# Performance work log

Hardware: AMD Instinct MI355X
Metric: run time of the kernel (lower is better)

The kernel has to match this reference:

```python
import jax, jax.numpy as jnp
import numpy as np

N_HEADS = 12
HEAD_DIM = 32
H_OUT = 28
W_OUT = 28
EPS_LN = 1e-6
EPS_TS = 1e-6


def _layer_norm(x, g, eps=EPS_LN):
    mu = jnp.mean(x, axis=-1, keepdims=True)
    xc = x - mu
    var = jnp.mean(xc * xc, axis=-1, keepdims=True)
    return xc * jax.lax.rsqrt(var + eps) * g


def setup_inputs() -> dict:
    key = jax.random.key(0)
    ks = jax.random.split(key, 6)
    b, hh, ww, d = 4, 56, 56, 384
    nc = 2 * H_OUT * W_OUT  # 1568
    s = 0.02
    return {
        "x": jax.random.normal(ks[0], (b, hh, ww, d), jnp.float32),
        "clusters": jax.random.normal(ks[1], (b, nc, d), jnp.float32),
        "g1": jnp.ones((d,), jnp.float32),
        "Wq": jax.random.normal(ks[2], (d, d), jnp.float32) * s,
        "Wkv": jax.random.normal(ks[3], (d, 2 * d), jnp.float32) * s,
        "Wo": jax.random.normal(ks[4], (d, d), jnp.float32) * s,
        "res_scale": jnp.ones((d,), jnp.float32),
        "g2": jnp.ones((2 * d,), jnp.float32),
        "Wproj": jax.random.normal(ks[5], (2 * d, 768), jnp.float32) * s,
    }


def reference(x, clusters, g1, Wq, Wkv, Wo, res_scale, g2, Wproj):
    b, hh, ww, d = x.shape
    n = hh * ww
    nc = clusters.shape[1]
    dh = HEAD_DIM
    scale = dh ** -0.5

    xf = x.reshape(b, n, d)
    xn = _layer_norm(xf, g1)
    cn = _layer_norm(clusters, g1)

    # projections; rearrange 'b n (h d) -> b h n d' and 'b n (k h d) -> k b h n d'
    q = (cn @ Wq).reshape(b, nc, N_HEADS, dh).transpose(0, 2, 1, 3)
    kv = (xn @ Wkv).reshape(b, n, 2, N_HEADS, dh)
    k = kv[:, :, 0].transpose(0, 2, 1, 3)  # [b h n dh]
    v = kv[:, :, 1].transpose(0, 2, 1, 3)

    attn = jnp.einsum('bhqd,bhkd->bhqk', q, k) * scale  # [b h nc n]
    # soft assignment: softmax over the query (cluster) axis
    attn = jax.nn.softmax(attn, axis=-2)
    token_sizes = attn.sum(-1)  # [b h nc]
    attn = attn / (token_sizes[..., None] + EPS_TS)
    token_sizes = token_sizes.mean(1)  # [b nc]

    c2 = jnp.einsum('bhqk,bhkd->bhqd', attn, v)
    c2 = c2.transpose(0, 2, 1, 3).reshape(b, nc, d) @ Wo

    token_sizes = token_sizes.reshape(b, nc // 2, 2).sum(-1)  # [b n']

    y = clusters * res_scale + c2
    y = y.reshape(b, nc // 2, 2 * d)  # 'b (n two) d -> b n (two d)'
    y = _layer_norm(y, g2) @ Wproj
    y = y.reshape(b, H_OUT, W_OUT, -1)
    token_sizes = token_sizes.reshape(b, H_OUT, W_OUT)
    return y, token_sizes
```

## Files before the change

kernel.cpp:

```cpp
#include <hip/hip_runtime.h>
#include <hip/hip_bf16.h>

typedef __hip_bfloat16 bf16;
typedef __attribute__((ext_vector_type(8))) short short8;
typedef __attribute__((ext_vector_type(4))) float f32x4;

#define B 4
#define NT 3136
#define NC 1568
#define NP 784
#define DMODEL 384
#define D2 768
#define NH 12
#define DH 32
#define SCALE 0.17677669529663687f
#define LOG2E 1.4426950408889634f
#define EPS_LN 1e-6f
#define EPS_TS 1e-6f

#if __has_builtin(__builtin_amdgcn_exp2f)
#define EXP2(x) __builtin_amdgcn_exp2f(x)
#else
#define EXP2(x) __expf(0.6931471805599453f * (x))
#endif

__device__ __forceinline__ unsigned short f2bf(float f) {
  return (unsigned short)(__bfloat16_as_ushort(__float2bfloat16(f)));
}
__device__ __forceinline__ float b2f(unsigned short u) {
  return __uint_as_float(((unsigned int)u) << 16);
}

__device__ __forceinline__ float lda(const void* __restrict__ p, size_t i,
                                     int mode, bool inf32) {
  bool f32 = (mode == 2) || (mode == 1 && inf32);
  return f32 ? ((const float*)p)[i]
             : __bfloat162float(((const bf16*)p)[i]);
}
__device__ __forceinline__ float4 lda4(const void* __restrict__ p, size_t i,
                                       int mode, bool inf32) {
  bool f32 = (mode == 2) || (mode == 1 && inf32);
  if (f32) return *(const float4*)((const float*)p + i);
  ushort4 u = *(const ushort4*)((const bf16*)p + i);
  return make_float4(b2f(u.x), b2f(u.y), b2f(u.z), b2f(u.w));
}

__global__ void sniff_kernel(const unsigned short* __restrict__ g1,
                             int* __restrict__ flag) {
  if (threadIdx.x == 0 && blockIdx.x == 0)
    *flag = (g1[0] == 0x3F80) ? 0 : 1;
}

__global__ void transpose_kernel(const void* __restrict__ in,
                                 const int* __restrict__ dtf,
                                 bf16* __restrict__ out, int K, int N,
                                 float scale) {
  bool inf32 = (*dtf != 0);
  __shared__ float t[32][33];
  int n0 = blockIdx.x * 32, k0 = blockIdx.y * 32;
  int tx = threadIdx.x & 31, ty = threadIdx.x >> 5;
#pragma unroll
  for (int s = 0; s < 32; s += 8)
    t[ty + s][tx] = lda(in, (size_t)(k0 + ty + s) * N + n0 + tx, 1, inf32);
  __syncthreads();
#pragma unroll
  for (int s = 0; s < 32; s += 8)
    out[(size_t)(n0 + ty + s) * K + k0 + tx] =
        __float2bfloat16(t[tx][ty + s] * scale);
}

__global__ void stats_kernel(const void* __restrict__ in, int mode,
                             const int* __restrict__ dtf,
                             float* __restrict__ stats, int D) {
  bool inf32 = (*dtf != 0);
  int row = blockIdx.x;
  int tid = threadIdx.x;
  size_t base = (size_t)row * D;
  int nper = D >> 7;
  float s = 0.f, s2 = 0.f;
  for (int i = 0; i < nper; i++) {
    float xv = lda(in, base + tid + (i << 7), mode, inf32);
    s += xv; s2 += xv * xv;
  }
  __shared__ float red[128], red2[128];
  red[tid] = s; red2[tid] = s2;
  __syncthreads();
  for (int off = 64; off > 0; off >>= 1) {
    if (tid < off) { red[tid] += red[tid + off]; red2[tid] += red2[tid + off]; }
    __syncthreads();
  }
  if (tid == 0) {
    float mean = red[0] / (float)D;
    float var  = red2[0] / (float)D - mean * mean;
    stats[row * 2]     = mean;
    stats[row * 2 + 1] = rsqrtf(var + EPS_LN);
  }
}

__global__ void __launch_bounds__(256, 3)
mgemm_kernel(const void* __restrict__ A, int a_mode, size_t a_bstr,
             const float* __restrict__ Astats, size_t s_bstr,
             const void* __restrict__ gammaA,
             const bf16* __restrict__ BT,
             const int* __restrict__ dtf,
             void* __restrict__ C, int c_f32, size_t c_bstr,
             bf16* __restrict__ Cv,
             int M, int N, int K,
             int epi,
             const void* __restrict__ resid, size_t r_bstr,
             const void* __restrict__ rscale) {
  bool inf32 = (*dtf != 0);
  int z = blockIdx.z;
  size_t a_off = (size_t)z * a_bstr;
  size_t r_off = (size_t)z * r_bstr;
  const float* st = Astats ? Astats + (size_t)z * s_bstr : nullptr;
  __shared__ __align__(16) unsigned short Asl[128][40];
  __shared__ __align__(16) unsigned short Bsl[128][40];
  int tid = threadIdx.x;
  int wave = tid >> 6, lane = tid & 63, l16 = lane & 15, quad = lane >> 4;
  int brow = blockIdx.y * 128, bcol = blockIdx.x * 128;
  int wm = (wave >> 1) * 64, wn = (wave & 1) * 64;
  f32x4 acc[4][4];
#pragma unroll
  for (int i = 0; i < 4; i++)
#pragma unroll
    for (int j = 0; j < 4; j++) acc[i][j] = (f32x4){0.f, 0.f, 0.f, 0.f};

  for (int k0 = 0; k0 < K; k0 += 32) {
#pragma unroll
    for (int it = 0; it < 4; it++) {
      int i = it * 256 + tid;
      int r = i >> 3, c4 = (i & 7) * 4;
      int grow = brow + r;
      if (grow >= M) grow = M - 1;
      float4 v = lda4(A, a_off + (size_t)grow * K + k0 + c4, a_mode, inf32);
      if (st) {
        float mu = st[grow * 2], rstd = st[grow * 2 + 1];
        float4 g = lda4(gammaA, k0 + c4, 1, inf32);
        v.x = (v.x - mu) * rstd * g.x; v.y = (v.y - mu) * rstd * g.y;
        v.z = (v.z - mu) * rstd * g.z; v.w = (v.w - mu) * rstd * g.w;
      }
      ushort4 u = {f2bf(v.x), f2bf(v.y), f2bf(v.z), f2bf(v.w)};
      *(ushort4*)&Asl[r][c4] = u;
    }
#pragma unroll
    for (int it = 0; it < 4; it++) {
      int i = it * 256 + tid;
      int r = i >> 3, c4 = (i & 7) * 4;
      *(ushort4*)&Bsl[r][c4] =
          *(const ushort4*)(BT + (size_t)(bcol + r) * K + k0 + c4);
    }
    __syncthreads();
    short8 af[4], bfr[4];
#pragma unroll
    for (int i = 0; i < 4; i++)
      af[i] = *(const short8*)&Asl[wm + 16 * i + l16][quad * 8];
#pragma unroll
    for (int j = 0; j < 4; j++)
      bfr[j] = *(const short8*)&Bsl[wn + 16 * j + l16][quad * 8];
#pragma unroll
    for (int i = 0; i < 4; i++)
#pragma unroll
      for (int j = 0; j < 4; j++)
        acc[i][j] = __builtin_amdgcn_mfma_f32_16x16x32_bf16(
            af[i], bfr[j], acc[i][j], 0, 0, 0);
    __syncthreads();
  }
#pragma unroll
  for (int i = 0; i < 4; i++) {
#pragma unroll
    for (int r = 0; r < 4; r++) {
      int m = brow + wm + 16 * i + quad * 4 + r;
      if (m < M) {
#pragma unroll
        for (int j = 0; j < 4; j++) {
          int n = bcol + wn + 16 * j + l16;
          float v = acc[i][j][r];
          if (epi == 1)
            v += lda(resid, r_off + (size_t)m * N + n, 1, inf32) *
                 lda(rscale, n, 1, inf32);
          if (epi == 2) {
            if (n < DMODEL) {
              ((bf16*)C)[(size_t)z * c_bstr + (size_t)m * DMODEL + n] =
                  __float2bfloat16(v);
            } else {
              int cc = n - DMODEL, hh = cc >> 5, dd = cc & 31;
              int w = m & 31;
              int pos = ((w >> 2) & 3) * 8 + (w >> 4) * 4 + (w & 3);
              Cv[(((size_t)z * NH + hh) * DH + dd) * NT + (m & ~31) + pos] =
                  __float2bfloat16(v);
            }
          } else {
            size_t idx = (size_t)z * c_bstr + (size_t)m * N + n;
            if (c_f32) ((float*)C)[idx] = v;
            else       ((bf16*)C)[idx]  = __float2bfloat16(v);
          }
        }
      }
    }
  }
}

__global__ void __launch_bounds__(256, 4)
colsum_mfma(const bf16* __restrict__ qm, const bf16* __restrict__ km,
            float* __restrict__ l2ci) {
  int b = blockIdx.z, h = blockIdx.y;
  int tid = threadIdx.x;
  int wave = tid >> 6, lane = tid & 63, l16 = lane & 15, quad = lane >> 4;
  int key0 = blockIdx.x * 128 + wave * 32 + l16;
  int key1 = key0 + 16;
  int kc0 = (key0 < NT) ? key0 : NT - 1;
  int kc1 = (key1 < NT) ? key1 : NT - 1;
  short8 kf0 = *(const short8*)(km +
      ((size_t)(b * NT + kc0) * DMODEL + h * DH + quad * 8));
  short8 kf1 = *(const short8*)(km +
      ((size_t)(b * NT + kc1) * DMODEL + h * DH + quad * 8));
  __shared__ __align__(16) unsigned short Qlds[32][40];
  const bf16* qb = qm + (size_t)b * NC * DMODEL + h * DH;
  int srow = tid >> 3, sc4 = (tid & 7) * 4;
  float cs0 = 0.f, cs1 = 0.f;
  for (int q0 = 0; q0 < NC; q0 += 32) {
    ushort4 qu = *(const ushort4*)(qb + (size_t)(q0 + srow) * DMODEL + sc4);
    __syncthreads();
    *(ushort4*)&Qlds[srow][sc4] = qu;
    __syncthreads();
    short8 a1 = *(const short8*)&Qlds[l16][quad * 8];
    short8 a2 = *(const short8*)&Qlds[16 + l16][quad * 8];
    f32x4 z = {0.f, 0.f, 0.f, 0.f};
    f32x4 s10 = __builtin_amdgcn_mfma_f32_16x16x32_bf16(a1, kf0, z, 0, 0, 0);
    f32x4 s20 = __builtin_amdgcn_mfma_f32_16x16x32_bf16(a2, kf0, z, 0, 0, 0);
    f32x4 s11 = __builtin_amdgcn_mfma_f32_16x16x32_bf16(a1, kf1, z, 0, 0, 0);
    f32x4 s21 = __builtin_amdgcn_mfma_f32_16x16x32_bf16(a2, kf1, z, 0, 0, 0);
#pragma unroll
    for (int r = 0; r < 4; r++) {
      cs0 += EXP2(s10[r]) + EXP2(s20[r]);
      cs1 += EXP2(s11[r]) + EXP2(s21[r]);
    }
  }
  cs0 += __shfl_xor(cs0, 16, 64);
  cs0 += __shfl_xor(cs0, 32, 64);
  cs1 += __shfl_xor(cs1, 16, 64);
  cs1 += __shfl_xor(cs1, 32, 64);
  if (quad == 0) {
    if (key0 < NT) l2ci[((size_t)b * NH + h) * NT + key0] = -__log2f(cs0);
    if (key1 < NT) l2ci[((size_t)b * NH + h) * NT + key1] = -__log2f(cs1);
  }
}

__global__ void __launch_bounds__(256, 4)
pv_mfma(const bf16* __restrict__ qm, const bf16* __restrict__ km,
        const bf16* __restrict__ vt, const float* __restrict__ l2ci,
        bf16* __restrict__ c2, float* __restrict__ rowsum) {
  int b = blockIdx.z, h = blockIdx.y;
  int tid = threadIdx.x;
  int wave = tid >> 6, lane = tid & 63, l16 = lane & 15, quad = lane >> 4;
  int q0w = blockIdx.x * 128 + wave * 32;
  short8 qfrag[2];
#pragma unroll
  for (int t = 0; t < 2; t++) {
    int qr = q0w + t * 16 + l16; if (qr >= NC) qr = NC - 1;
    qfrag[t] = *(const short8*)(qm +
        ((size_t)(b * NC + qr) * DMODEL + h * DH + quad * 8));
  }
  __shared__ __align__(16) unsigned short Klds[64][40];
  __shared__ __align__(16) unsigned short Vlds[32][72];
  __shared__ __align__(16) float csl[64];
  f32x4 olo[2], ohi[2];
#pragma unroll
  for (int t = 0; t < 2; t++) {
    olo[t] = (f32x4){0.f, 0.f, 0.f, 0.f};
    ohi[t] = (f32x4){0.f, 0.f, 0.f, 0.f};
  }
  float rs[2] = {0.f, 0.f};
  const float* csb = l2ci + ((size_t)b * NH + h) * NT;
  const bf16* kb = km + (size_t)b * NT * DMODEL + h * DH;
  const bf16* vtb = vt + ((size_t)b * NH + h) * DH * NT;
  int krow = tid >> 2, kc8 = (tid & 3) * 8;
  int vrow = tid >> 3, vc8 = (tid & 7) * 8;
  for (int k0 = 0; k0 < NT; k0 += 64) {
    short8 ku = *(const short8*)(kb + (size_t)(k0 + krow) * DMODEL + kc8);
    short8 vu = *(const short8*)(vtb + (size_t)vrow * NT + k0 + vc8);
    float4 cf;
    if (tid < 16) cf = *(const float4*)(csb + k0 + tid * 4);
    __syncthreads();
    *(short8*)&Klds[krow][kc8] = ku;
    *(short8*)&Vlds[vrow][vc8] = vu;
    if (tid < 16) *(float4*)&csl[tid * 4] = cf;
    __syncthreads();
#pragma unroll
    for (int ks = 0; ks < 64; ks += 32) {
      short8 kf1 = *(const short8*)&Klds[ks + l16][quad * 8];
      short8 kf2 = *(const short8*)&Klds[ks + 16 + l16][quad * 8];
      float4 ci1 = *(const float4*)&csl[ks + quad * 4];
      float4 ci2 = *(const float4*)&csl[ks + 16 + quad * 4];
      short8 vlo = *(const short8*)&Vlds[l16][ks + quad * 8];
      short8 vhi = *(const short8*)&Vlds[16 + l16][ks + quad * 8];
#pragma unroll
      for (int t = 0; t < 2; t++) {
        f32x4 z = {0.f, 0.f, 0.f, 0.f};
        f32x4 s1 = __builtin_amdgcn_mfma_f32_16x16x32_bf16(kf1, qfrag[t], z, 0, 0, 0);
        f32x4 s2 = __builtin_amdgcn_mfma_f32_16x16x32_bf16(kf2, qfrag[t], z, 0, 0, 0);
        float p0 = EXP2(s1[0] + ci1.x);
        float p1 = EXP2(s1[1] + ci1.y);
        float p2 = EXP2(s1[2] + ci1.z);
        float p3 = EXP2(s1[3] + ci1.w);
        float p4 = EXP2(s2[0] + ci2.x);
        float p5 = EXP2(s2[1] + ci2.y);
        float p6 = EXP2(s2[2] + ci2.z);
        float p7 = EXP2(s2[3] + ci2.w);
        rs[t] += ((p0 + p1) + (p2 + p3)) + ((p4 + p5) + (p6 + p7));
        short8 pf;
        pf[0] = (short)f2bf(p0); pf[1] = (short)f2bf(p1);
        pf[2] = (short)f2bf(p2); pf[3] = (short)f2bf(p3);
        pf[4] = (short)f2bf(p4); pf[5] = (short)f2bf(p5);
        pf[6] = (short)f2bf(p6); pf[7] = (short)f2bf(p7);
        olo[t] = __builtin_amdgcn_mfma_f32_16x16x32_bf16(pf, vlo, olo[t], 0, 0, 0);
        ohi[t] = __builtin_amdgcn_mfma_f32_16x16x32_bf16(pf, vhi, ohi[t], 0, 0, 0);
      }
    }
  }
  bf16* c2b = c2 + (size_t)b * NC * DMODEL + h * DH;
#pragma unroll
  for (int t = 0; t < 2; t++) {
    float v = rs[t];
    v += __shfl_xor(v, 16, 64);
    v += __shfl_xor(v, 32, 64);
    rs[t] = v;
#pragma unroll
    for (int r = 0; r < 4; r++) {
      int qloc = quad * 4 + r;
      float rsq = __shfl(rs[t], qloc, 64);
      int q = q0w + t * 16 + qloc;
      if (q < NC) {
        float inv = 1.0f / (rsq + EPS_TS);
        c2b[(size_t)q * DMODEL + l16]      = __float2bfloat16(olo[t][r] * inv);
        c2b[(size_t)q * DMODEL + 16 + l16] = __float2bfloat16(ohi[t][r] * inv);
      }
    }
    int qr = q0w + t * 16 + l16;
    if (quad == 0 && qr < NC)
      rowsum[((size_t)b * NH + h) * NC + qr] = rs[t];
  }
}

__global__ void tok_kernel(const float* __restrict__ rowsum,
                           float* __restrict__ out_ts) {
  int idx = blockIdx.x * 256 + threadIdx.x;
  if (idx >= B * NP) return;
  int b = idx / NP, p = idx % NP;
  float s = 0.f;
  for (int h = 0; h < NH; h++) {
    const float* r = rowsum + ((size_t)b * NH + h) * NC;
    s += r[2 * p] + r[2 * p + 1];
  }
  out_ts[idx] = s / (float)NH;
}

extern "C" void kernel_launch(void* const* d_in, const int* in_sizes, int n_in,
                              void* d_out, int out_size, void* d_ws, size_t ws_size,
                              hipStream_t stream) {
  const void* x         = d_in[0];
  const void* clusters  = d_in[1];
  const void* g1        = d_in[2];
  const void* Wq        = d_in[3];
  const void* Wkv       = d_in[4];
  const void* Wo        = d_in[5];
  const void* res_scale = d_in[6];
  const void* g2        = d_in[7];
  const void* Wproj     = d_in[8];
  float* out = (float*)d_out;

  float* fws = (float*)d_ws;
  size_t fo = 0;
  int*   dtf     = (int*)(fws + fo); fo += 4;
  float* stats_x = fws + fo; fo += (size_t)B * NT * 2;
  float* stats_c = fws + fo; fo += (size_t)B * NC * 2;
  float* stats_y = fws + fo; fo += (size_t)B * NP * 2;
  float* colsum  = fws + fo; fo += (size_t)B * NH * NT;
  float* rowsum  = fws + fo; fo += (size_t)B * NH * NC;
  float* y1f     = fws + fo; fo += (size_t)B * NC * DMODEL;
  fo = (fo + 3) & ~(size_t)3;
  bf16* bws = (bf16*)(fws + fo);
  size_t o = 0;
  bf16* qm     = bws + o; o += (size_t)B * NC * DMODEL;
  bf16* km     = bws + o; o += (size_t)B * NT * DMODEL;
  bf16* vt     = bws + o; o += (size_t)B * NH * DH * NT;
  bf16* c2     = bws + o; o += (size_t)B * NC * DMODEL;
  bf16* wqT    = bws + o; o += (size_t)DMODEL * DMODEL;
  bf16* wkvT   = bws + o; o += (size_t)DMODEL * D2;
  bf16* woT    = bws + o; o += (size_t)DMODEL * DMODEL;
  bf16* wprojT = bws + o; o += (size_t)D2 * D2;

  const size_t xstr = (size_t)NT * DMODEL, cstr = (size_t)NC * DMODEL;
  const size_t ystr = (size_t)NP * D2;

  sniff_kernel<<<1, 1, 0, stream>>>((const unsigned short*)g1, dtf);
  transpose_kernel<<<dim3(DMODEL / 32, DMODEL / 32), 256, 0, stream>>>(
      Wq, dtf, wqT, DMODEL, DMODEL, SCALE * LOG2E);
  transpose_kernel<<<dim3(D2 / 32, DMODEL / 32), 256, 0, stream>>>(
      Wkv, dtf, wkvT, DMODEL, D2, 1.0f);
  transpose_kernel<<<dim3(DMODEL / 32, DMODEL / 32), 256, 0, stream>>>(
      Wo, dtf, woT, DMODEL, DMODEL, 1.0f);
  transpose_kernel<<<dim3(D2 / 32, D2 / 32), 256, 0, stream>>>(
      Wproj, dtf, wprojT, D2, D2, 1.0f);
  stats_kernel<<<B * NT, 128, 0, stream>>>(x, 1, dtf, stats_x, DMODEL);
  stats_kernel<<<B * NC, 128, 0, stream>>>(clusters, 1, dtf, stats_c, DMODEL);

  mgemm_kernel<<<dim3(DMODEL / 128, (NC + 127) / 128, B), 256, 0, stream>>>(
      clusters, 1, cstr, stats_c, (size_t)NC * 2, g1, wqT, dtf,
      qm, 0, cstr, nullptr, NC, DMODEL, DMODEL, 0, nullptr, 0, nullptr);
  mgemm_kernel<<<dim3(D2 / 128, (NT + 127) / 128, B), 256, 0, stream>>>(
      x, 1, xstr, stats_x, (size_t)NT * 2, g1, wkvT, dtf,
      km, 0, xstr, vt, NT, D2, DMODEL, 2, nullptr, 0, nullptr);
  colsum_mfma<<<dim3((NT + 127) / 128, NH, B), 256, 0, stream>>>(qm, km, colsum);
  pv_mfma<<<dim3((NC + 127) / 128, NH, B), 256, 0, stream>>>(
      qm, km, vt, colsum, c2, rowsum);
  mgemm_kernel<<<dim3(DMODEL / 128, (NC + 127) / 128, B), 256, 0, stream>>>(
      c2, 0, cstr, nullptr, 0, nullptr, woT, dtf,
      y1f, 1, cstr, nullptr, NC, DMODEL, DMODEL, 1, clusters, cstr, res_scale);
  stats_kernel<<<B * NP, 128, 0, stream>>>(y1f, 2, dtf, stats_y, D2);
  mgemm_kernel<<<dim3(D2 / 128, (NP + 127) / 128, B), 256, 0, stream>>>(
      y1f, 2, cstr, stats_y, (size_t)NP * 2, g2, wprojT, dtf,
      out, 1, ystr, nullptr, NP, D2, D2, 0, nullptr, 0, nullptr);
  tok_kernel<<<(B * NP + 255) / 256, 256, 0, stream>>>(
      rowsum, out + (size_t)B * NP * D2);
}
```

Measured before the change: 415.1 us.

## Split pv_mfma key loop across waves with LDS reduction of partial outputs

The PV kernel now gives each block 32 queries instead of 128 and has its four waves split each 128-key tile between them (split-K inside the block). Partial outputs and row sums are then reduced through shared memory before wave 0 writes the result. The grid grows fourfold (49x12x4 blocks) and launch bounds rise to 8 blocks per CU, which targets low occupancy and a short wave count. In exchange, every block re-streams all keys and values for only 32 queries, so global/L2 traffic for K and V goes up fourfold, and a serialized per-wave reduction is added at the end.

```diff
diff --git a/kernel.cpp b/kernel.cpp
--- a/kernel.cpp
+++ b/kernel.cpp
@@ -247,24 +247,25 @@
   }
 }
 
-__global__ void __launch_bounds__(256, 4)
+__global__ void __launch_bounds__(256, 8)
 pv_mfma(const bf16* __restrict__ qm, const bf16* __restrict__ km,
         const bf16* __restrict__ vt, const float* __restrict__ l2ci,
         bf16* __restrict__ c2, float* __restrict__ rowsum) {
   int b = blockIdx.z, h = blockIdx.y;
   int tid = threadIdx.x;
   int wave = tid >> 6, lane = tid & 63, l16 = lane & 15, quad = lane >> 4;
-  int q0w = blockIdx.x * 128 + wave * 32;
+  int q0w = blockIdx.x * 32;
+  int ksb = wave * 32;
   short8 qfrag[2];
 #pragma unroll
   for (int t = 0; t < 2; t++) {
-    int qr = q0w + t * 16 + l16; if (qr >= NC) qr = NC - 1;
+    int qr = q0w + t * 16 + l16;
     qfrag[t] = *(const short8*)(qm +
         ((size_t)(b * NC + qr) * DMODEL + h * DH + quad * 8));
   }
-  __shared__ __align__(16) unsigned short Klds[64][40];
-  __shared__ __align__(16) unsigned short Vlds[32][72];
-  __shared__ __align__(16) float csl[64];
+  __shared__ __align__(16) unsigned short Klds[128][40];
+  __shared__ __align__(16) unsigned short Vlds[32][136];
+  __shared__ __align__(16) float csl[128];
   f32x4 olo[2], ohi[2];
 #pragma unroll
   for (int t = 0; t < 2; t++) {
@@ -275,71 +276,111 @@
   const float* csb = l2ci + ((size_t)b * NH + h) * NT;
   const bf16* kb = km + (size_t)b * NT * DMODEL + h * DH;
   const bf16* vtb = vt + ((size_t)b * NH + h) * DH * NT;
-  int krow = tid >> 2, kc8 = (tid & 3) * 8;
-  int vrow = tid >> 3, vc8 = (tid & 7) * 8;
-  for (int k0 = 0; k0 < NT; k0 += 64) {
-    short8 ku = *(const short8*)(kb + (size_t)(k0 + krow) * DMODEL + kc8);
-    short8 vu = *(const short8*)(vtb + (size_t)vrow * NT + k0 + vc8);
-    float4 cf;
-    if (tid < 16) cf = *(const float4*)(csb + k0 + tid * 4);
-    __syncthreads();
-    *(short8*)&Klds[krow][kc8] = ku;
-    *(short8*)&Vlds[vrow][vc8] = vu;
-    if (tid < 16) *(float4*)&csl[tid * 4] = cf;
-    __syncthreads();
-#pragma unroll
-    for (int ks = 0; ks < 64; ks += 32) {
-      short8 kf1 = *(const short8*)&Klds[ks + l16][quad * 8];
-      short8 kf2 = *(const short8*)&Klds[ks + 16 + l16][quad * 8];
-      float4 ci1 = *(const float4*)&csl[ks + quad * 4];
-      float4 ci2 = *(const float4*)&csl[ks + 16 + quad * 4];
-      short8 vlo = *(const short8*)&Vlds[l16][ks + quad * 8];
-      short8 vhi = *(const short8*)&Vlds[16 + l16][ks + quad * 8];
+  int krow = tid >> 1, kc = (tid & 1) * 16;
+  int vrow = tid >> 3, vc = (tid & 7) * 16;
+  const short8 z8 = {0, 0, 0, 0, 0, 0, 0, 0};
+  for (int k0 = 0; k0 < NT; k0 += 128) {
+    short8 ku0 = z8, ku1 = z8, vu0 = z8, vu1 = z8;
+    if (k0 + krow < NT) {
+      const bf16* kr = kb + (size_t)(k0 + krow) * DMODEL + kc;
+      ku0 = *(const short8*)kr;
+      ku1 = *(const short8*)(kr + 8);
+    }
+    {
+      const bf16* vr = vtb + (size_t)vrow * NT + k0 + vc;
+      if (k0 + vc + 8 <= NT)  vu0 = *(const short8*)vr;
+      if (k0 + vc + 16 <= NT) vu1 = *(const short8*)(vr + 8);
+    }
+    float4 cf = make_float4(-1e30f, -1e30f, -1e30f, -1e30f);
+    if (tid < 32) {
+      int cidx = k0 + tid * 4;
+      if (cidx + 4 <= NT) cf = *(const float4*)(csb + cidx);
+    }
+    __syncthreads();
+    *(short8*)&Klds[krow][kc] = ku0;
+    *(short8*)&Klds[krow][kc + 8] = ku1;
+    *(short8*)&Vlds[vrow][vc] = vu0;
+    *(short8*)&Vlds[vrow][vc + 8] = vu1;
+    if (tid < 32) *(float4*)&csl[tid * 4] = cf;
+    __syncthreads();
+    short8 kf1 = *(const short8*)&Klds[ksb + l16][quad * 8];
+    short8 kf2 = *(const short8*)&Klds[ksb + 16 + l16][quad * 8];
+    float4 ci1 = *(const float4*)&csl[ksb + quad * 4];
+    float4 ci2 = *(const float4*)&csl[ksb + 16 + quad * 4];
+    short8 vlo = *(const short8*)&Vlds[l16][ksb + quad * 8];
+    short8 vhi = *(const short8*)&Vlds[16 + l16][ksb + quad * 8];
+#pragma unroll
+    for (int t = 0; t < 2; t++) {
+      f32x4 z = {0.f, 0.f, 0.f, 0.f};
+      f32x4 s1 = __builtin_amdgcn_mfma_f32_16x16x32_bf16(kf1, qfrag[t], z, 0, 0, 0);
+      f32x4 s2 = __builtin_amdgcn_mfma_f32_16x16x32_bf16(kf2, qfrag[t], z, 0, 0, 0);
+      float p0 = EXP2(s1[0] + ci1.x);
+      float p1 = EXP2(s1[1] + ci1.y);
+      float p2 = EXP2(s1[2] + ci1.z);
+      float p3 = EXP2(s1[3] + ci1.w);
+      float p4 = EXP2(s2[0] + ci2.x);
+      float p5 = EXP2(s2[1] + ci2.y);
+      float p6 = EXP2(s2[2] + ci2.z);
+      float p7 = EXP2(s2[3] + ci2.w);
+      rs[t] += ((p0 + p1) + (p2 + p3)) + ((p4 + p5) + (p6 + p7));
+      short8 pf;
+      pf[0] = (short)f2bf(p0); pf[1] = (short)f2bf(p1);
+      pf[2] = (short)f2bf(p2); pf[3] = (short)f2bf(p3);
+      pf[4] = (short)f2bf(p4); pf[5] = (short)f2bf(p5);
+      pf[6] = (short)f2bf(p6); pf[7] = (short)f2bf(p7);
+      olo[t] = __builtin_amdgcn_mfma_f32_16x16x32_bf16(pf, vlo, olo[t], 0, 0, 0);
+      ohi[t] = __builtin_amdgcn_mfma_f32_16x16x32_bf16(pf, vhi, ohi[t], 0, 0, 0);
+    }
+  }
+#pragma unroll
+  for (int t = 0; t < 2; t++) {
+    rs[t] += __shfl_xor(rs[t], 16, 64);
+    rs[t] += __shfl_xor(rs[t], 32, 64);
+  }
+  __syncthreads();
+  float* redO = (float*)&Klds[0][0];
+  float* redR = (float*)&Vlds[0][0];
+  for (int w = 0; w < 4; w++) {
+    if (wave == w) {
 #pragma unroll
       for (int t = 0; t < 2; t++) {
-        f32x4 z = {0.f, 0.f, 0.f, 0.f};
-        f32x4 s1 = __builtin_amdgcn_mfma_f32_16x16x32_bf16(kf1, qfrag[t], z, 0, 0, 0);
-        f32x4 s2 = __builtin_amdgcn_mfma_f32_16x16x32_bf16(kf2, qfrag[t], z, 0, 0, 0);
-        float p0 = EXP2(s1[0] + ci1.x);
-        float p1 = EXP2(s1[1] + ci1.y);
-        float p2 = EXP2(s1[2] + ci1.z);
-        float p3 = EXP2(s1[3] + ci1.w);
-        float p4 = EXP2(s2[0] + ci2.x);
-        float p5 = EXP2(s2[1] + ci2.y);
-        float p6 = EXP2(s2[2] + ci2.z);
-        float p7 = EXP2(s2[3] + ci2.w);
-        rs[t] += ((p0 + p1) + (p2 + p3)) + ((p4 + p5) + (p6 + p7));
-        short8 pf;
-        pf[0] = (short)f2bf(p0); pf[1] = (short)f2bf(p1);
-        pf[2] = (short)f2bf(p2); pf[3] = (short)f2bf(p3);
-        pf[4] = (short)f2bf(p4); pf[5] = (short)f2bf(p5);
-        pf[6] = (short)f2bf(p6); pf[7] = (short)f2bf(p7);
-        olo[t] = __builtin_amdgcn_mfma_f32_16x16x32_bf16(pf, vlo, olo[t], 0, 0, 0);
-        ohi[t] = __builtin_amdgcn_mfma_f32_16x16x32_bf16(pf, vhi, ohi[t], 0, 0, 0);
+#pragma unroll
+        for (int r = 0; r < 4; r++) {
+          int qloc = t * 16 + quad * 4 + r;
+          if (w == 0) {
+            redO[qloc * 32 + l16]      = olo[t][r];
+            redO[qloc * 32 + 16 + l16] = ohi[t][r];
+          } else {
+            redO[qloc * 32 + l16]      += olo[t][r];
+            redO[qloc * 32 + 16 + l16] += ohi[t][r];
+          }
+        }
+        if (quad == 0) {
+          if (w == 0) redR[t * 16 + l16]  = rs[t];
+          else        redR[t * 16 + l16] += rs[t];
+        }
       }
     }
-  }
-  bf16* c2b = c2 + (size_t)b * NC * DMODEL + h * DH;
-#pragma unroll
-  for (int t = 0; t < 2; t++) {
-    float v = rs[t];
-    v += __shfl_xor(v, 16, 64);
-    v += __shfl_xor(v, 32, 64);
-    rs[t] = v;
-#pragma unroll
-    for (int r = 0; r < 4; r++) {
-      int qloc = quad * 4 + r;
-      float rsq = __shfl(rs[t], qloc, 64);
-      int q = q0w + t * 16 + qloc;
-      if (q < NC) {
-        float inv = 1.0f / (rsq + EPS_TS);
-        c2b[(size_t)q * DMODEL + l16]      = __float2bfloat16(olo[t][r] * inv);
-        c2b[(size_t)q * DMODEL + 16 + l16] = __float2bfloat16(ohi[t][r] * inv);
+    __syncthreads();
+  }
+  if (wave == 0) {
+    bf16* c2b = c2 + (size_t)b * NC * DMODEL + h * DH;
+#pragma unroll
+    for (int t = 0; t < 2; t++) {
+#pragma unroll
+      for (int r = 0; r < 4; r++) {
+        int qloc = t * 16 + quad * 4 + r;
+        int q = q0w + qloc;
+        float inv = 1.0f / (redR[qloc] + EPS_TS);
+        c2b[(size_t)q * DMODEL + l16] =
+            __float2bfloat16(redO[qloc * 32 + l16] * inv);
+        c2b[(size_t)q * DMODEL + 16 + l16] =
+            __float2bfloat16(redO[qloc * 32 + 16 + l16] * inv);
       }
-    }
-    int qr = q0w + t * 16 + l16;
-    if (quad == 0 && qr < NC)
-      rowsum[((size_t)b * NH + h) * NC + qr] = rs[t];
+      if (quad == 0)
+        rowsum[((size_t)b * NH + h) * NC + q0w + t * 16 + l16] =
+            redR[t * 16 + l16];
+    }
   }
 }
 
@@ -413,7 +454,7 @@
       x, 1, xstr, stats_x, (size_t)NT * 2, g1, wkvT, dtf,
       km, 0, xstr, vt, NT, D2, DMODEL, 2, nullptr, 0, nullptr);
   colsum_mfma<<<dim3((NT + 127) / 128, NH, B), 256, 0, stream>>>(qm, km, colsum);
-  pv_mfma<<<dim3((NC + 127) / 128, NH, B), 256, 0, stream>>>(
+  pv_mfma<<<dim3(NC / 32, NH, B), 256, 0, stream>>>(
       qm, km, vt, colsum, c2, rowsum);
   mgemm_kernel<<<dim3(DMODEL / 128, (NC + 127) / 128, B), 256, 0, stream>>>(
       c2, 0, cstr, nullptr, 0, nullptr, woT, dtf,
```

After: 510.0 us. 1.23x slower.

## Split PV attention over key range with separate combine kernel

Applied to the files above, without the earlier changes.

Splits the PV attention kernel's key loop into two halves launched as separate blocks, doubling the grid to improve CU occupancy. Each block writes unnormalized fp32 partial outputs and row sums. A new combine kernel sums them, normalizes, and writes bf16 c2. Launch bounds are raised to allow more resident blocks. This adds extra global traffic for the partials and one more kernel launch.

```diff
diff --git a/kernel.cpp b/kernel.cpp
--- a/kernel.cpp
+++ b/kernel.cpp
@@ -13,6 +13,8 @@
 #define D2 768
 #define NH 12
 #define DH 32
+#define KSPLIT 2
+#define KSPLIT0 1600
 #define SCALE 0.17677669529663687f
 #define LOG2E 1.4426950408889634f
 #define EPS_LN 1e-6f
@@ -247,11 +249,13 @@
   }
 }
 
-__global__ void __launch_bounds__(256, 4)
+__global__ void __launch_bounds__(256, 8)
 pv_mfma(const bf16* __restrict__ qm, const bf16* __restrict__ km,
         const bf16* __restrict__ vt, const float* __restrict__ l2ci,
-        bf16* __restrict__ c2, float* __restrict__ rowsum) {
-  int b = blockIdx.z, h = blockIdx.y;
+        float* __restrict__ po, float* __restrict__ prs) {
+  int z = blockIdx.z;
+  int b = z >> 1, split = z & 1;
+  int h = blockIdx.y;
   int tid = threadIdx.x;
   int wave = tid >> 6, lane = tid & 63, l16 = lane & 15, quad = lane >> 4;
   int q0w = blockIdx.x * 128 + wave * 32;
@@ -277,7 +281,9 @@
   const bf16* vtb = vt + ((size_t)b * NH + h) * DH * NT;
   int krow = tid >> 2, kc8 = (tid & 3) * 8;
   int vrow = tid >> 3, vc8 = (tid & 7) * 8;
-  for (int k0 = 0; k0 < NT; k0 += 64) {
+  int kbeg = split ? KSPLIT0 : 0;
+  int kend = split ? NT : KSPLIT0;
+  for (int k0 = kbeg; k0 < kend; k0 += 64) {
     short8 ku = *(const short8*)(kb + (size_t)(k0 + krow) * DMODEL + kc8);
     short8 vu = *(const short8*)(vtb + (size_t)vrow * NT + k0 + vc8);
     float4 cf;
@@ -297,9 +303,9 @@
       short8 vhi = *(const short8*)&Vlds[16 + l16][ks + quad * 8];
 #pragma unroll
       for (int t = 0; t < 2; t++) {
-        f32x4 z = {0.f, 0.f, 0.f, 0.f};
-        f32x4 s1 = __builtin_amdgcn_mfma_f32_16x16x32_bf16(kf1, qfrag[t], z, 0, 0, 0);
-        f32x4 s2 = __builtin_amdgcn_mfma_f32_16x16x32_bf16(kf2, qfrag[t], z, 0, 0, 0);
+        f32x4 z4 = {0.f, 0.f, 0.f, 0.f};
+        f32x4 s1 = __builtin_amdgcn_mfma_f32_16x16x32_bf16(kf1, qfrag[t], z4, 0, 0, 0);
+        f32x4 s2 = __builtin_amdgcn_mfma_f32_16x16x32_bf16(kf2, qfrag[t], z4, 0, 0, 0);
         float p0 = EXP2(s1[0] + ci1.x);
         float p1 = EXP2(s1[1] + ci1.y);
         float p2 = EXP2(s1[2] + ci1.z);
@@ -319,39 +325,55 @@
       }
     }
   }
-  bf16* c2b = c2 + (size_t)b * NC * DMODEL + h * DH;
 #pragma unroll
   for (int t = 0; t < 2; t++) {
-    float v = rs[t];
-    v += __shfl_xor(v, 16, 64);
-    v += __shfl_xor(v, 32, 64);
-    rs[t] = v;
+    rs[t] += __shfl_xor(rs[t], 16, 64);
+    rs[t] += __shfl_xor(rs[t], 32, 64);
+  }
+  size_t pb = ((size_t)(split * B + b) * NH + h) * NC;
+#pragma unroll
+  for (int t = 0; t < 2; t++) {
 #pragma unroll
     for (int r = 0; r < 4; r++) {
       int qloc = quad * 4 + r;
-      float rsq = __shfl(rs[t], qloc, 64);
       int q = q0w + t * 16 + qloc;
       if (q < NC) {
-        float inv = 1.0f / (rsq + EPS_TS);
-        c2b[(size_t)q * DMODEL + l16]      = __float2bfloat16(olo[t][r] * inv);
-        c2b[(size_t)q * DMODEL + 16 + l16] = __float2bfloat16(ohi[t][r] * inv);
+        po[(pb + q) * 32 + l16]      = olo[t][r];
+        po[(pb + q) * 32 + 16 + l16] = ohi[t][r];
       }
     }
     int qr = q0w + t * 16 + l16;
-    if (quad == 0 && qr < NC)
-      rowsum[((size_t)b * NH + h) * NC + qr] = rs[t];
-  }
-}
-
-__global__ void tok_kernel(const float* __restrict__ rowsum,
+    if (quad == 0 && qr < NC) prs[pb + qr] = rs[t];
+  }
+}
+
+__global__ void combine_kernel(const float* __restrict__ po,
+                               const float* __restrict__ prs,
+                               bf16* __restrict__ c2) {
+  int bh = blockIdx.y;
+  int tid = threadIdx.x;
+  int q = blockIdx.x * 8 + (tid >> 5);
+  int d = tid & 31;
+  int b = bh / NH, h = bh - b * NH;
+  size_t base0 = (size_t)bh * NC;
+  size_t base1 = (size_t)B * NH * NC + base0;
+  float o = po[(base0 + q) * 32 + d] + po[(base1 + q) * 32 + d];
+  float rs = prs[base0 + q] + prs[base1 + q];
+  c2[((size_t)b * NC + q) * DMODEL + h * 32 + d] =
+      __float2bfloat16(o / (rs + EPS_TS));
+}
+
+__global__ void tok_kernel(const float* __restrict__ prs,
                            float* __restrict__ out_ts) {
   int idx = blockIdx.x * 256 + threadIdx.x;
   if (idx >= B * NP) return;
   int b = idx / NP, p = idx % NP;
   float s = 0.f;
   for (int h = 0; h < NH; h++) {
-    const float* r = rowsum + ((size_t)b * NH + h) * NC;
-    s += r[2 * p] + r[2 * p + 1];
+    size_t b0 = ((size_t)b * NH + h) * NC;
+    size_t b1 = (size_t)B * NH * NC + b0;
+    s += prs[b0 + 2 * p] + prs[b0 + 2 * p + 1] +
+         prs[b1 + 2 * p] + prs[b1 + 2 * p + 1];
   }
   out_ts[idx] = s / (float)NH;
 }
@@ -377,8 +399,9 @@
   float* stats_c = fws + fo; fo += (size_t)B * NC * 2;
   float* stats_y = fws + fo; fo += (size_t)B * NP * 2;
   float* colsum  = fws + fo; fo += (size_t)B * NH * NT;
-  float* rowsum  = fws + fo; fo += (size_t)B * NH * NC;
-  float* y1f     = fws + fo; fo += (size_t)B * NC * DMODEL;
+  float* prs     = fws + fo; fo += (size_t)KSPLIT * B * NH * NC;
+  float* po      = fws + fo; fo += (size_t)KSPLIT * B * NC * DMODEL;
+  float* y1f     = po;
   fo = (fo + 3) & ~(size_t)3;
   bf16* bws = (bf16*)(fws + fo);
   size_t o = 0;
@@ -413,8 +436,9 @@
       x, 1, xstr, stats_x, (size_t)NT * 2, g1, wkvT, dtf,
       km, 0, xstr, vt, NT, D2, DMODEL, 2, nullptr, 0, nullptr);
   colsum_mfma<<<dim3((NT + 127) / 128, NH, B), 256, 0, stream>>>(qm, km, colsum);
-  pv_mfma<<<dim3((NC + 127) / 128, NH, B), 256, 0, stream>>>(
-      qm, km, vt, colsum, c2, rowsum);
+  pv_mfma<<<dim3((NC + 127) / 128, NH, B * KSPLIT), 256, 0, stream>>>(
+      qm, km, vt, colsum, po, prs);
+  combine_kernel<<<dim3(NC / 8, B * NH), 256, 0, stream>>>(po, prs, c2);
   mgemm_kernel<<<dim3(DMODEL / 128, (NC + 127) / 128, B), 256, 0, stream>>>(
       c2, 0, cstr, nullptr, 0, nullptr, woT, dtf,
       y1f, 1, cstr, nullptr, NC, DMODEL, DMODEL, 1, clusters, cstr, res_scale);
@@ -423,5 +447,5 @@
       y1f, 2, cstr, stats_y, (size_t)NP * 2, g2, wprojT, dtf,
       out, 1, ystr, nullptr, NP, D2, D2, 0, nullptr, 0, nullptr);
   tok_kernel<<<(B * NP + 255) / 256, 256, 0, stream>>>(
-      rowsum, out + (size_t)B * NP * D2);
-}
+      prs, out + (size_t)B * NP * D2);
+}
```

Result: slower. 555.9 us (+33.9%).
